# Kernel optimization log

Hardware: AMD Instinct MI355X
Metric: run time of the kernel (lower is better)

Reference implementation:

```python
import jax, jax.numpy as jnp
import numpy as np

GRID_SIZE = 5
SPLINE_ORDER = 3
GRID_LO, GRID_HI = -1.0, 1.0
N_COEFF = GRID_SIZE + SPLINE_ORDER  # 8


def make_grid(in_features):
    # (in_features, grid_size + 2*spline_order + 1) = (in, 12)
    h = (GRID_HI - GRID_LO) / GRID_SIZE
    g = jnp.arange(-SPLINE_ORDER, GRID_SIZE + SPLINE_ORDER + 1, dtype=jnp.float32) * h + GRID_LO
    return jnp.broadcast_to(g, (in_features, g.shape[0]))


def b_splines(x, grid):
    # x: (N, in); grid: (in, G). Returns (N, in, grid_size+spline_order).
    xe = x[..., None]
    bases = ((xe >= grid[:, :-1]) & (xe < grid[:, 1:])).astype(x.dtype)
    for k in range(1, SPLINE_ORDER + 1):
        left = (xe - grid[:, :-(k + 1)]) / (grid[:, k:-1] - grid[:, :-(k + 1)]) * bases[..., :-1]
        right = (grid[:, k + 1:] - xe) / (grid[:, k + 1:] - grid[:, 1:-k]) * bases[..., 1:]
        bases = left + right
    return bases


def kan_linear(x, base_w, spline_w, scaler, grid):
    # base branch: SiLU(x) @ base_w^T
    base_out = jax.nn.silu(x) @ base_w.T
    # spline branch: basis (N,in,c) contracted with scaled spline weight (out,in,c)
    b = b_splines(x, grid)
    sw = spline_w * scaler[..., None]
    spline_out = jnp.einsum('nic,oic->no', b, sw)
    return base_out + spline_out


def setup_inputs() -> dict:
    key = jax.random.key(0)
    ks = jax.random.split(key, 7)
    d_model, d_hid = 512, 2049  # d_ff + 1
    s = 0.1  # keep activations roughly inside grid range
    return {
        "x": jax.random.normal(ks[0], (4096, d_model), dtype=jnp.float32) * 0.3,
        "base_w1": jax.random.normal(ks[1], (d_hid, d_model), dtype=jnp.float32) * s,
        "spline_w1": jax.random.normal(ks[2], (d_hid, d_model, N_COEFF), dtype=jnp.float32) * s,
        "scaler1": jax.random.normal(ks[3], (d_hid, d_model), dtype=jnp.float32) * s,
        "base_w2": jax.random.normal(ks[4], (d_model, d_hid), dtype=jnp.float32) * s,
        "spline_w2": jax.random.normal(ks[5], (d_model, d_hid, N_COEFF), dtype=jnp.float32) * s,
        "scaler2": jax.random.normal(ks[6], (d_model, d_hid), dtype=jnp.float32) * s,
    }


def reference(x, base_w1, spline_w1, scaler1, base_w2, spline_w2, scaler2):
    grid1 = make_grid(x.shape[-1])
    h = kan_linear(x, base_w1, spline_w1, scaler1, grid1)
    grid2 = make_grid(h.shape[-1])
    out = kan_linear(h, base_w2, spline_w2, scaler2, grid2)
    return out
```

## Files before the change

### kernel.cpp

```cpp
#include <hip/hip_runtime.h>
#include <hip/hip_bf16.h>

#define T_TOK 4096
#define I1    512
#define O1    2049
#define O1P   2176
#define K1    4608
#define G1    64
#define I2    2049
#define O2    512
#define K2    18560
#define G2    271
#define SPLITS2 8
#define KLEN2 2368
#define NBY   32

typedef __attribute__((ext_vector_type(8))) short short8;
typedef __attribute__((ext_vector_type(4))) float floatx4;
typedef __attribute__((address_space(3))) void* lds_ptr_t;
typedef const __attribute__((address_space(1))) void* gmem_ptr_t;

__device__ __forceinline__ unsigned short f2bf(float f) {
  union { __hip_bfloat16 h; unsigned short u; } cv;
  cv.h = __float2bfloat16(f);
  return cv.u;
}
__device__ __forceinline__ unsigned bfr(float f) {
  union { float f; unsigned u; } c; c.f = f;
  return (c.u + 0x8000u) >> 16;
}
__device__ __forceinline__ float silu_f(float x) { return x / (1.0f + __expf(-x)); }

__device__ __forceinline__ uint4 spline_pack(float h) {
  float u = (h + 2.2f) * 2.5f;
  int ji = (int)u;
  ji = ji < 0 ? 0 : (ji > 10 ? 10 : ji);
  float t = u - (float)ji;
  float it = 1.0f - t, t2 = t * t, t3 = t2 * t;
  float b0 = it * it * it * (1.0f / 6.0f);
  float b1 = (3.0f * t3 - 6.0f * t2 + 4.0f) * (1.0f / 6.0f);
  float b2 = (-3.0f * t3 + 3.0f * t2 + 3.0f * t + 1.0f) * (1.0f / 6.0f);
  float b3 = t3 * (1.0f / 6.0f);
  unsigned pk01 = bfr(b0) | (bfr(b1) << 16);
  unsigned pk23 = bfr(b2) | (bfr(b3) << 16);
  unsigned long long p64 = (unsigned long long)pk01 | ((unsigned long long)pk23 << 32);
  bool inR = (h >= -2.2f) && (h < 2.2f);
  p64 = inR ? p64 : 0ull;
  int sh = (ji - 3) * 16;
  int shr = sh < 0 ? -sh : 0;
  int shl = sh < 0 ? 0 : sh;
  __uint128_t v = ((__uint128_t)(p64 >> shr)) << shl;
  union { __uint128_t q; uint4 u4; } cv;
  cv.q = v;
  return cv.u4;
}

__global__ void transpose_kernel(const float* __restrict__ src, float* __restrict__ dst,
                                 int R, int C) {
  __shared__ float t[32][33];
  int c0 = blockIdx.x * 32, r0 = blockIdx.y * 32;
  int tx = threadIdx.x & 31, ty = threadIdx.x >> 5;
#pragma unroll
  for (int i = 0; i < 32; i += 8)
    t[ty + i][tx] = src[(size_t)(r0 + ty + i) * C + c0 + tx];
  __syncthreads();
#pragma unroll
  for (int i = 0; i < 32; i += 8)
    dst[(size_t)(c0 + ty + i) * R + r0 + tx] = t[tx][ty + i];
}

__global__ void silu_pack_kernel(const float* __restrict__ St, uint4* __restrict__ SPK,
                                 int I, int M) {
  int m = blockIdx.x * 256 + threadIdx.x;
  int g = blockIdx.y;
  int off0 = g * 8;
  union { unsigned short s[8]; uint4 v; } pk;
#pragma unroll
  for (int c = 0; c < 8; ++c) {
    int off = off0 + c;
    float v = 0.0f;
    if (off < I) v = silu_f(St[(size_t)off * M + m]);
    pk.s[c] = f2bf(v);
  }
  SPK[(size_t)g * M + m] = pk.v;
}

__global__ void pack_w1_kernel(const float* __restrict__ bw, const float* __restrict__ sw,
                               const float* __restrict__ sc, unsigned short* __restrict__ W) {
  int k = blockIdx.x * 256 + threadIdx.x;
  int o = blockIdx.y;
  float v = 0.0f;
  if (o < O1) {
    if (k < 4096) v = sw[(size_t)o * 4096 + k] * sc[(size_t)o * I1 + (k >> 3)];
    else          v = bw[(size_t)o * I1 + (k - 4096)];
  }
  W[(size_t)o * K1 + k] = f2bf(v);
}

__global__ void pack_w2_kernel(const float* __restrict__ bw, const float* __restrict__ sw,
                               const float* __restrict__ sc, unsigned short* __restrict__ W) {
  int k = blockIdx.x * 256 + threadIdx.x;
  if (k >= K2) return;
  int o = blockIdx.y;
  float v = 0.0f;
  if (k < 16392)      v = sw[(size_t)o * 16392 + k] * sc[(size_t)o * I2 + (k >> 3)];
  else if (k < 18441) v = bw[(size_t)o * I2 + (k - 16392)];
  W[(size_t)o * K2 + k] = f2bf(v);
}

__global__ __launch_bounds__(256, 4)
void kan_gemm_kernel(const float* __restrict__ St, const uint4* __restrict__ SPK,
                     const unsigned short* __restrict__ Bw, float* __restrict__ C,
                     int I, int Ktot, int M, int N, int ldc, int kLen,
                     int nBx, int storeMode)
{
  __shared__ __align__(16) unsigned short As[128 * 64];
  __shared__ __align__(16) unsigned short Bs[128 * 64];

  const int Lb = blockIdx.x;
  const int m8 = Lb & 7;
  const int r  = Lb >> 3;
  const int bx = r % nBx;
  const int p  = m8 + ((r / nBx) << 3);
  const int by = p & (NBY - 1);
  const int bz = p >> 5;

  const int tid = threadIdx.x;
  const int ks = bz * kLen;
  int ke = ks + kLen; if (ke > Ktot) ke = Ktot;

  const int w = tid >> 6, L = tid & 63, q = L >> 4, ln = L & 15;
  const int wm = (w & 1) << 6, wn = (w >> 1) << 6;

  const int row = tid & 127;
  const int gh  = tid >> 7;
  const int mGlob = by * 128 + row;
  const float* s0  = St + mGlob;
  const uint4* sp0 = SPK + mGlob;

  floatx4 zf = {0.f, 0.f, 0.f, 0.f};
  floatx4 acc[4][4];
#pragma unroll
  for (int mt = 0; mt < 4; ++mt)
#pragma unroll
    for (int nt = 0; nt < 4; ++nt)
      acc[mt][nt] = zf;

  const unsigned short* gb[4];
  int ldsOff[4];
#pragma unroll
  for (int r4 = 0; r4 < 4; ++r4) {
    int e = r4 * 256 + tid;
    int br = e >> 3;
    int cg = (e & 7) ^ (br & 7);
    gb[r4] = Bw + ((long)bx * 128 + br) * (long)Ktot + ks + cg * 8;
    ldsOff[r4] = e * 8;
  }

  uint4 cur[4], nxt[4];
#pragma unroll
  for (int j2 = 0; j2 < 4; ++j2) {
    int gi = (ks >> 3) + gh * 4 + j2;
    if (gi < I) cur[j2].x = __float_as_uint(s0[(size_t)gi * M]);
    else        cur[j2]   = sp0[(size_t)(gi - I) * M];
  }

  for (int kc = ks; kc < ke; kc += 64) {
    __syncthreads();
#pragma unroll
    for (int r4 = 0; r4 < 4; ++r4) {
      __builtin_amdgcn_global_load_lds((gmem_ptr_t)gb[r4], (lds_ptr_t)&Bs[ldsOff[r4]], 16, 0, 0);
      gb[r4] += 64;
    }
    if (kc + 64 < ke) {
#pragma unroll
      for (int j2 = 0; j2 < 4; ++j2) {
        int gi = ((kc + 64) >> 3) + gh * 4 + j2;
        if (gi < I) nxt[j2].x = __float_as_uint(s0[(size_t)gi * M]);
        else        nxt[j2]   = sp0[(size_t)(gi - I) * M];
      }
    }

    const int gBase = (kc >> 3) + gh * 4;
#pragma unroll
    for (int j2 = 0; j2 < 4; ++j2) {
      int g  = gh * 4 + j2;
      int gi = gBase + j2;
      int pos = row * 64 + ((g ^ (row & 7)) << 3);
      uint4 val;
      if (gi < I) val = spline_pack(__uint_as_float(cur[j2].x));
      else        val = cur[j2];
      *(uint4*)&As[pos] = val;
    }
    __syncthreads();

#pragma unroll
    for (int s = 0; s < 2; ++s) {
      short8 af[4], bf[4];
#pragma unroll
      for (int mt = 0; mt < 4; ++mt) {
        int rr = wm + mt * 16 + ln;
        int cl = ((s << 2) | q) ^ (rr & 7);
        af[mt] = *(const short8*)&As[rr * 64 + cl * 8];
      }
#pragma unroll
      for (int nt = 0; nt < 4; ++nt) {
        int rr = wn + nt * 16 + ln;
        int cl = ((s << 2) | q) ^ (rr & 7);
        bf[nt] = *(const short8*)&Bs[rr * 64 + cl * 8];
      }
#pragma unroll
      for (int mt = 0; mt < 4; ++mt)
#pragma unroll
        for (int nt = 0; nt < 4; ++nt)
          acc[mt][nt] = __builtin_amdgcn_mfma_f32_16x16x32_bf16(af[mt], bf[nt], acc[mt][nt], 0, 0, 0);
    }
#pragma unroll
    for (int j2 = 0; j2 < 4; ++j2) cur[j2] = nxt[j2];
  }

  if (storeMode == 1) {
#pragma unroll
    for (int mt = 0; mt < 4; ++mt) {
#pragma unroll
      for (int nt = 0; nt < 4; ++nt) {
        int n = bx * 128 + wn + nt * 16 + ln;
        if (n < N) {
          int m0 = by * 128 + wm + mt * 16 + q * 4;
          *(float4*)&C[(size_t)n * ldc + m0] = *(float4*)&acc[mt][nt];
        }
      }
    }
  } else {
#pragma unroll
    for (int mt = 0; mt < 4; ++mt) {
#pragma unroll
      for (int nt = 0; nt < 4; ++nt) {
        int n = bx * 128 + wn + nt * 16 + ln;
        if (n < N) {
          int m0 = by * 128 + wm + mt * 16 + q * 4;
#pragma unroll
          for (int rg = 0; rg < 4; ++rg)
            atomicAdd(&C[(size_t)(m0 + rg) * ldc + n], acc[mt][nt][rg]);
        }
      }
    }
  }
}

extern "C" void kernel_launch(void* const* d_in, const int* in_sizes, int n_in,
                              void* d_out, int out_size, void* d_ws, size_t ws_size,
                              hipStream_t stream) {
  const float* x   = (const float*)d_in[0];
  const float* bw1 = (const float*)d_in[1];
  const float* sw1 = (const float*)d_in[2];
  const float* sc1 = (const float*)d_in[3];
  const float* bw2 = (const float*)d_in[4];
  const float* sw2 = (const float*)d_in[5];
  const float* sc2 = (const float*)d_in[6];
  float* out = (float*)d_out;

  float* Xt  = (float*)d_ws;
  float* H0t = Xt + (size_t)I1 * T_TOK;
  unsigned short* W1 = (unsigned short*)(H0t + (size_t)O1 * T_TOK);
  unsigned short* W2 = W1 + (size_t)O1P * K1;
  uint4* SPK1 = (uint4*)(W2 + (size_t)O2 * K2);
  uint4* SPK2 = SPK1 + (size_t)G1 * T_TOK;

  hipMemsetAsync(d_out, 0, (size_t)out_size * sizeof(float), stream);

  transpose_kernel<<<dim3(I1 / 32, T_TOK / 32), 256, 0, stream>>>(x, Xt, T_TOK, I1);
  pack_w1_kernel<<<dim3(K1 / 256, O1P), 256, 0, stream>>>(bw1, sw1, sc1, W1);
  pack_w2_kernel<<<dim3((K2 + 255) / 256, O2), 256, 0, stream>>>(bw2, sw2, sc2, W2);
  silu_pack_kernel<<<dim3(T_TOK / 256, G1), 256, 0, stream>>>(Xt, SPK1, I1, T_TOK);

  kan_gemm_kernel<<<O1P / 128 * NBY, 256, 0, stream>>>(
      Xt, SPK1, W1, H0t, I1, K1, T_TOK, O1, T_TOK, K1, O1P / 128, 1);

  silu_pack_kernel<<<dim3(T_TOK / 256, G2), 256, 0, stream>>>(H0t, SPK2, I2, T_TOK);

  kan_gemm_kernel<<<O2 / 128 * NBY * SPLITS2, 256, 0, stream>>>(
      H0t, SPK2, W2, out, I2, K2, T_TOK, O2, O2, KLEN2, O2 / 128, 2);
}
```

Before: 503.3 us.

## Materialize expanded spline/SiLU activations in global memory and use plain BF16 GEMM

Replaces the in-GEMM on-the-fly B-spline expansion (which read transposed fp32 activations and computed basis values per tile) with separate expand kernels that write the full bf16 A matrices (spline bases plus SiLU) row-major. The GEMM then loads both A and B straight into LDS with global_load_lds, which removes per-tile ALU work and the register prefetch path. It also drops the transpose kernel and stores H row-major. The cost is much more global memory traffic: A2 alone is about 4096x18560 bf16 written and then reread, and the first GEMM's stores become scalar and strided.

```diff
diff --git a/kernel.cpp b/kernel.cpp
--- a/kernel.cpp
+++ b/kernel.cpp
@@ -6,11 +6,12 @@
 #define O1    2049
 #define O1P   2176
 #define K1    4608
-#define G1    64
+#define NG1   576
 #define I2    2049
 #define O2    512
 #define K2    18560
-#define G2    271
+#define NG2   2320
+#define HLD   2176
 #define SPLITS2 8
 #define KLEN2 2368
 #define NBY   32
@@ -55,36 +56,6 @@
   return cv.u4;
 }
 
-__global__ void transpose_kernel(const float* __restrict__ src, float* __restrict__ dst,
-                                 int R, int C) {
-  __shared__ float t[32][33];
-  int c0 = blockIdx.x * 32, r0 = blockIdx.y * 32;
-  int tx = threadIdx.x & 31, ty = threadIdx.x >> 5;
-#pragma unroll
-  for (int i = 0; i < 32; i += 8)
-    t[ty + i][tx] = src[(size_t)(r0 + ty + i) * C + c0 + tx];
-  __syncthreads();
-#pragma unroll
-  for (int i = 0; i < 32; i += 8)
-    dst[(size_t)(c0 + ty + i) * R + r0 + tx] = t[tx][ty + i];
-}
-
-__global__ void silu_pack_kernel(const float* __restrict__ St, uint4* __restrict__ SPK,
-                                 int I, int M) {
-  int m = blockIdx.x * 256 + threadIdx.x;
-  int g = blockIdx.y;
-  int off0 = g * 8;
-  union { unsigned short s[8]; uint4 v; } pk;
-#pragma unroll
-  for (int c = 0; c < 8; ++c) {
-    int off = off0 + c;
-    float v = 0.0f;
-    if (off < I) v = silu_f(St[(size_t)off * M + m]);
-    pk.s[c] = f2bf(v);
-  }
-  SPK[(size_t)g * M + m] = pk.v;
-}
-
 __global__ void pack_w1_kernel(const float* __restrict__ bw, const float* __restrict__ sw,
                                const float* __restrict__ sc, unsigned short* __restrict__ W) {
   int k = blockIdx.x * 256 + threadIdx.x;
@@ -108,11 +79,53 @@
   W[(size_t)o * K2 + k] = f2bf(v);
 }
 
+__global__ void expand1_kernel(const float* __restrict__ x, unsigned short* __restrict__ A) {
+  int g = blockIdx.x * 256 + threadIdx.x;
+  if (g >= NG1) return;
+  int m = blockIdx.y;
+  uint4 val;
+  if (g < 512) {
+    val = spline_pack(x[(size_t)m * I1 + g]);
+  } else {
+    const float4* xr = (const float4*)(x + (size_t)m * I1 + (size_t)(g - 512) * 8);
+    float4 a = xr[0], b = xr[1];
+    union { unsigned short s[8]; uint4 v; } pk;
+    pk.s[0] = f2bf(silu_f(a.x)); pk.s[1] = f2bf(silu_f(a.y));
+    pk.s[2] = f2bf(silu_f(a.z)); pk.s[3] = f2bf(silu_f(a.w));
+    pk.s[4] = f2bf(silu_f(b.x)); pk.s[5] = f2bf(silu_f(b.y));
+    pk.s[6] = f2bf(silu_f(b.z)); pk.s[7] = f2bf(silu_f(b.w));
+    val = pk.v;
+  }
+  *(uint4*)(A + (size_t)m * K1 + (size_t)g * 8) = val;
+}
+
+__global__ void expand2_kernel(const float* __restrict__ H, unsigned short* __restrict__ A) {
+  int g = blockIdx.x * 256 + threadIdx.x;
+  if (g >= NG2) return;
+  int m = blockIdx.y;
+  uint4 val;
+  if (g < 2049) {
+    val = spline_pack(H[(size_t)m * HLD + g]);
+  } else if (g < 2306) {
+    int c0 = (g - 2049) * 8;
+    union { unsigned short s[8]; uint4 v; } pk;
+#pragma unroll
+    for (int c = 0; c < 8; ++c) {
+      int idx = c0 + c;
+      float v = (idx < I2) ? silu_f(H[(size_t)m * HLD + idx]) : 0.0f;
+      pk.s[c] = f2bf(v);
+    }
+    val = pk.v;
+  } else {
+    val = make_uint4(0u, 0u, 0u, 0u);
+  }
+  *(uint4*)(A + (size_t)m * K2 + (size_t)g * 8) = val;
+}
+
 __global__ __launch_bounds__(256, 4)
-void kan_gemm_kernel(const float* __restrict__ St, const uint4* __restrict__ SPK,
-                     const unsigned short* __restrict__ Bw, float* __restrict__ C,
-                     int I, int Ktot, int M, int N, int ldc, int kLen,
-                     int nBx, int storeMode)
+void gemm_bt_kernel(const unsigned short* __restrict__ Aw, const unsigned short* __restrict__ Bw,
+                    float* __restrict__ C, int Ktot, int N, int ldc, int kLen,
+                    int nBx, int storeMode)
 {
   __shared__ __align__(16) unsigned short As[128 * 64];
   __shared__ __align__(16) unsigned short Bs[128 * 64];
@@ -132,12 +145,6 @@
   const int w = tid >> 6, L = tid & 63, q = L >> 4, ln = L & 15;
   const int wm = (w & 1) << 6, wn = (w >> 1) << 6;
 
-  const int row = tid & 127;
-  const int gh  = tid >> 7;
-  const int mGlob = by * 128 + row;
-  const float* s0  = St + mGlob;
-  const uint4* sp0 = SPK + mGlob;
-
   floatx4 zf = {0.f, 0.f, 0.f, 0.f};
   floatx4 acc[4][4];
 #pragma unroll
@@ -146,6 +153,7 @@
     for (int nt = 0; nt < 4; ++nt)
       acc[mt][nt] = zf;
 
+  const unsigned short* ga[4];
   const unsigned short* gb[4];
   int ldsOff[4];
 #pragma unroll
@@ -153,44 +161,19 @@
     int e = r4 * 256 + tid;
     int br = e >> 3;
     int cg = (e & 7) ^ (br & 7);
+    ga[r4] = Aw + ((long)by * 128 + br) * (long)Ktot + ks + cg * 8;
     gb[r4] = Bw + ((long)bx * 128 + br) * (long)Ktot + ks + cg * 8;
     ldsOff[r4] = e * 8;
   }
 
-  uint4 cur[4], nxt[4];
-#pragma unroll
-  for (int j2 = 0; j2 < 4; ++j2) {
-    int gi = (ks >> 3) + gh * 4 + j2;
-    if (gi < I) cur[j2].x = __float_as_uint(s0[(size_t)gi * M]);
-    else        cur[j2]   = sp0[(size_t)(gi - I) * M];
-  }
-
   for (int kc = ks; kc < ke; kc += 64) {
     __syncthreads();
 #pragma unroll
     for (int r4 = 0; r4 < 4; ++r4) {
+      __builtin_amdgcn_global_load_lds((gmem_ptr_t)ga[r4], (lds_ptr_t)&As[ldsOff[r4]], 16, 0, 0);
+      ga[r4] += 64;
       __builtin_amdgcn_global_load_lds((gmem_ptr_t)gb[r4], (lds_ptr_t)&Bs[ldsOff[r4]], 16, 0, 0);
       gb[r4] += 64;
-    }
-    if (kc + 64 < ke) {
-#pragma unroll
-      for (int j2 = 0; j2 < 4; ++j2) {
-        int gi = ((kc + 64) >> 3) + gh * 4 + j2;
-        if (gi < I) nxt[j2].x = __float_as_uint(s0[(size_t)gi * M]);
-        else        nxt[j2]   = sp0[(size_t)(gi - I) * M];
-      }
-    }
-
-    const int gBase = (kc >> 3) + gh * 4;
-#pragma unroll
-    for (int j2 = 0; j2 < 4; ++j2) {
-      int g  = gh * 4 + j2;
-      int gi = gBase + j2;
-      int pos = row * 64 + ((g ^ (row & 7)) << 3);
-      uint4 val;
-      if (gi < I) val = spline_pack(__uint_as_float(cur[j2].x));
-      else        val = cur[j2];
-      *(uint4*)&As[pos] = val;
     }
     __syncthreads();
 
@@ -215,11 +198,9 @@
         for (int nt = 0; nt < 4; ++nt)
           acc[mt][nt] = __builtin_amdgcn_mfma_f32_16x16x32_bf16(af[mt], bf[nt], acc[mt][nt], 0, 0, 0);
     }
-#pragma unroll
-    for (int j2 = 0; j2 < 4; ++j2) cur[j2] = nxt[j2];
-  }
-
-  if (storeMode == 1) {
+  }
+
+  if (storeMode == 0) {
 #pragma unroll
     for (int mt = 0; mt < 4; ++mt) {
 #pragma unroll
@@ -227,7 +208,9 @@
         int n = bx * 128 + wn + nt * 16 + ln;
         if (n < N) {
           int m0 = by * 128 + wm + mt * 16 + q * 4;
-          *(float4*)&C[(size_t)n * ldc + m0] = *(float4*)&acc[mt][nt];
+#pragma unroll
+          for (int rg = 0; rg < 4; ++rg)
+            C[(size_t)(m0 + rg) * ldc + n] = acc[mt][nt][rg];
         }
       }
     }
@@ -260,25 +243,23 @@
   const float* sc2 = (const float*)d_in[6];
   float* out = (float*)d_out;
 
-  float* Xt  = (float*)d_ws;
-  float* H0t = Xt + (size_t)I1 * T_TOK;
-  unsigned short* W1 = (unsigned short*)(H0t + (size_t)O1 * T_TOK);
-  unsigned short* W2 = W1 + (size_t)O1P * K1;
-  uint4* SPK1 = (uint4*)(W2 + (size_t)O2 * K2);
-  uint4* SPK2 = SPK1 + (size_t)G1 * T_TOK;
+  float* H = (float*)d_ws;
+  unsigned short* W2 = (unsigned short*)(H + (size_t)T_TOK * HLD);
+  unsigned short* A2 = W2 + (size_t)O2 * K2;
+  unsigned short* A1 = A2;
+  unsigned short* W1 = A1 + (size_t)T_TOK * K1;
 
   hipMemsetAsync(d_out, 0, (size_t)out_size * sizeof(float), stream);
 
-  transpose_kernel<<<dim3(I1 / 32, T_TOK / 32), 256, 0, stream>>>(x, Xt, T_TOK, I1);
   pack_w1_kernel<<<dim3(K1 / 256, O1P), 256, 0, stream>>>(bw1, sw1, sc1, W1);
   pack_w2_kernel<<<dim3((K2 + 255) / 256, O2), 256, 0, stream>>>(bw2, sw2, sc2, W2);
-  silu_pack_kernel<<<dim3(T_TOK / 256, G1), 256, 0, stream>>>(Xt, SPK1, I1, T_TOK);
-
-  kan_gemm_kernel<<<O1P / 128 * NBY, 256, 0, stream>>>(
-      Xt, SPK1, W1, H0t, I1, K1, T_TOK, O1, T_TOK, K1, O1P / 128, 1);
-
-  silu_pack_kernel<<<dim3(T_TOK / 256, G2), 256, 0, stream>>>(H0t, SPK2, I2, T_TOK);
-
-  kan_gemm_kernel<<<O2 / 128 * NBY * SPLITS2, 256, 0, stream>>>(
-      H0t, SPK2, W2, out, I2, K2, T_TOK, O2, O2, KLEN2, O2 / 128, 2);
-}
+  expand1_kernel<<<dim3((NG1 + 255) / 256, T_TOK), 256, 0, stream>>>(x, A1);
+
+  gemm_bt_kernel<<<(O1P / 128) * NBY, 256, 0, stream>>>(
+      A1, W1, H, K1, O1, HLD, K1, O1P / 128, 0);
+
+  expand2_kernel<<<dim3((NG2 + 255) / 256, T_TOK), 256, 0, stream>>>(H, A2);
+
+  gemm_bt_kernel<<<(O2 / 128) * NBY * SPLITS2, 256, 0, stream>>>(
+      A2, W2, out, K2, O2, O2, KLEN2, O2 / 128, 2);
+}
```

After: 411.0 us. 18.3% less time.
